# Optimization experiments

Measured on AMD Instinct MI355X. Metric: run time of the kernel, lower is better.

Reference implementation:

```python
import jax, jax.numpy as jnp
import numpy as np

N_NODES = 100000
N_EDGES = 3200000
IN_CH = 256
HIDDEN = 64
OUT_CH = 128


def setup_inputs() -> dict:
    key = jax.random.key(0)
    ks = jax.random.split(key, 6)
    x = jax.random.normal(ks[0], (N_NODES, IN_CH), dtype=jnp.float32)
    edge_index = jax.random.randint(ks[1], (2, N_EDGES), 0, N_NODES, dtype=jnp.int64)
    W1 = jax.random.normal(ks[2], (IN_CH, HIDDEN), dtype=jnp.float32) * (1.0 / np.sqrt(IN_CH))
    b1 = jnp.zeros((HIDDEN,), dtype=jnp.float32)
    W2 = jax.random.normal(ks[3], (HIDDEN, OUT_CH), dtype=jnp.float32) * (1.0 / np.sqrt(HIDDEN))
    b2 = jnp.zeros((OUT_CH,), dtype=jnp.float32)
    fcW = jax.random.normal(ks[4], (2, OUT_CH), dtype=jnp.float32) * (1.0 / np.sqrt(OUT_CH))
    fcb = jnp.zeros((2,), dtype=jnp.float32)
    return {"x": x, "edge_index": edge_index, "W1": W1, "b1": b1,
            "W2": W2, "b2": b2, "fcW": fcW, "fcb": fcb}


def _gcn_conv(x, edge_index, W, b):
    """PyG GCNConv: linear transform, add self-loops, symmetric D^-1/2 A D^-1/2 aggregation, bias."""
    N = x.shape[0]
    h = x @ W  # [N, F_out]
    loops = jnp.arange(N, dtype=edge_index.dtype)
    row = jnp.concatenate([edge_index[0], loops])  # source nodes
    col = jnp.concatenate([edge_index[1], loops])  # destination nodes
    deg = jax.ops.segment_sum(jnp.ones_like(col, dtype=h.dtype), col, num_segments=N)
    dinv = jnp.where(deg > 0, jax.lax.rsqrt(deg), 0.0)
    norm = dinv[row] * dinv[col]  # [E+N]
    out = jax.ops.segment_sum(h[row] * norm[:, None], col, num_segments=N)
    return out + b


def reference(x, edge_index, W1, b1, W2, b2, fcW, fcb):
    h = jax.nn.relu(_gcn_conv(x, edge_index, W1, b1))
    h = jax.nn.relu(_gcn_conv(h, edge_index, W2, b2))
    g = jnp.mean(h, axis=0)  # [OUT_CH]
    return g @ fcW.T + fcb   # [2]
```

## Files before the change

### kernel.cpp

```cpp
#include <hip/hip_runtime.h>

#define N_NODES 100000
#define N_EDGES 3200000
#define C_IN 256
#define C_H 64
#define C_OUT 128
#define NB 391
#define BCAP 16384
#define G2F 625
#define NTILES 6250
#define NT16 6250
#define G_GM 1563
#define CH1 8192

typedef unsigned int u32;
typedef unsigned short u16;
typedef unsigned long long u64;
typedef __attribute__((ext_vector_type(8))) short bf16x8;
typedef __attribute__((ext_vector_type(4))) float f32x4;

typedef __attribute__((address_space(3))) unsigned int l_u32;
typedef __attribute__((address_space(1))) const unsigned int g_u32;

__device__ __forceinline__ float bf2f(u16 u) {
    union { u32 i; float f; } v; v.i = ((u32)u) << 16; return v.f;
}
__device__ __forceinline__ u16 f2bf(float f) {
    union { float f; u32 i; } v; v.f = f;
    u32 x = v.i;
    return (u16)((x + 0x7fffu + ((x >> 16) & 1u)) >> 16);
}

__device__ __forceinline__ void gll16(const void* gp, const u16* lp) {
    __builtin_amdgcn_global_load_lds((g_u32*)gp, (l_u32*)lp, 16, 0, 0);
}

__global__ void k_detect(const void* __restrict__ x, const void* __restrict__ ei,
                         const void* __restrict__ b1, const void* __restrict__ b2,
                         const void* __restrict__ fcW, const void* __restrict__ fcb,
                         int* __restrict__ flags,
                         float* __restrict__ b1c, float* __restrict__ b2c,
                         float* __restrict__ fcWc, float* __restrict__ fcbc) {
    __shared__ int sf[2];
    int t = threadIdx.x;
    if (t < 64) {
        u32 w = ((const u32*)x)[t];
        u32 low = w & 0xffffu;
        int e = (int)((low >> 7) & 0xff);
        bool inw = (e > 96 && e < 160) || (low == 0);
        u64 m = __ballot(inw);
        if (t == 0) sf[0] = (__popcll(m) >= 60) ? 1 : 0;
    } else if (t < 128) {
        int i = t - 64;
        u32 w = ((const u32*)ei)[2 * i + 1];
        u64 m = __ballot(w == 0);
        if (i == 0) sf[1] = (m == ~0ull) ? 1 : 0;
    }
    __syncthreads();
    if (t == 0) { flags[0] = sf[0]; flags[1] = sf[1]; }
    int isbf = sf[0];
    if (isbf) {
        const u16* p1 = (const u16*)b1;  const u16* p2 = (const u16*)b2;
        const u16* pw = (const u16*)fcW; const u16* pb = (const u16*)fcb;
        for (int i = t; i < C_H; i += 256) b1c[i] = bf2f(p1[i]);
        for (int i = t; i < C_OUT; i += 256) b2c[i] = bf2f(p2[i]);
        for (int i = t; i < 2 * C_OUT; i += 256) fcWc[i] = bf2f(pw[i]);
        for (int i = t; i < 2; i += 256) fcbc[i] = bf2f(pb[i]);
    } else {
        const float* p1 = (const float*)b1;  const float* p2 = (const float*)b2;
        const float* pw = (const float*)fcW; const float* pb = (const float*)fcb;
        for (int i = t; i < C_H; i += 256) b1c[i] = p1[i];
        for (int i = t; i < C_OUT; i += 256) b2c[i] = p2[i];
        for (int i = t; i < 2 * C_OUT; i += 256) fcWc[i] = pw[i];
        for (int i = t; i < 2; i += 256) fcbc[i] = pb[i];
    }
}

__global__ __launch_bounds__(256) void k_prep(const void* __restrict__ W1,
                                              const void* __restrict__ W2,
                                              const int* __restrict__ flags,
                                              u16* __restrict__ W1m, u16* __restrict__ W2m,
                                              u32* __restrict__ bucket_cnt) {
    int b = blockIdx.x, t = threadIdx.x;
    int isbf = flags[0];
    int i = b * 256 + t;
    if (i < NB) bucket_cnt[i] = 0;
    if (i < C_IN * C_H) {
        const u16* w1b = (const u16*)W1; const float* w1f = (const float*)W1;
        int j = i & 7, lane = (i >> 3) & 63, nt = (i >> 9) & 3, k0 = i >> 11;
        int k = k0 * 32 + ((lane >> 4) & 3) * 8 + j;
        int n = nt * 16 + (lane & 15);
        W1m[i] = isbf ? w1b[k * C_H + n] : f2bf(w1f[k * C_H + n]);
    } else {
        int i2 = i - C_IN * C_H;
        const u16* w2b = (const u16*)W2; const float* w2f = (const float*)W2;
        int j = i2 & 7, lane = (i2 >> 3) & 63, nt = (i2 >> 9) & 7, k0 = (i2 >> 12) & 1;
        int k = k0 * 32 + ((lane >> 4) & 3) * 8 + j;
        int n = nt * 16 + (lane & 15);
        W2m[i2] = isbf ? w2b[k * C_OUT + n] : f2bf(w2f[k * C_OUT + n]);
    }
}

__global__ __launch_bounds__(512) void k_scatter1(const int* __restrict__ ei,
                                                  const int* __restrict__ flags,
                                                  u32* __restrict__ bucket_cnt,
                                                  u32* __restrict__ ebuf) {
    __shared__ u32 cnt[NB];
    __shared__ u32 lcur[NB];
    __shared__ u32 gbase[NB];
    __shared__ u32 lofs[512];
    __shared__ u32 stp[CH1];
    __shared__ u16 stb[CH1];
    int t = threadIdx.x;
    int is64 = flags[1];
    int e0 = blockIdx.x * CH1;
    int nv = min(CH1, N_EDGES - e0);
    for (int i = t; i < NB; i += 512) { cnt[i] = 0; lcur[i] = 0; }
    __syncthreads();
    for (int i = t; i < nv; i += 512) {
        int e = e0 + i;
        int d = is64 ? ei[2 * (N_EDGES + e)] : ei[N_EDGES + e];
        atomicAdd(&cnt[d >> 8], 1u);
    }
    __syncthreads();
    u32 v = (t < NB) ? cnt[t] : 0;
    lofs[t] = v;
    __syncthreads();
    for (int off = 1; off < 512; off <<= 1) {
        u32 a = (t >= off) ? lofs[t - off] : 0;
        __syncthreads();
        lofs[t] += a;
        __syncthreads();
    }
    u32 excl = lofs[t] - v;
    __syncthreads();
    lofs[t] = excl;
    __syncthreads();
    for (int i = t; i < nv; i += 512) {
        int e = e0 + i;
        int d, s;
        if (is64) { d = ei[2 * (N_EDGES + e)]; s = ei[2 * e]; }
        else      { d = ei[N_EDGES + e];       s = ei[e]; }
        int b = d >> 8;
        u32 slot = lofs[b] + atomicAdd(&lcur[b], 1u);
        stp[slot] = ((u32)(d & 255) << 20) | (u32)s;
        stb[slot] = (u16)b;
    }
    __syncthreads();
    for (int b = t; b < NB; b += 512) {
        u32 c = cnt[b];
        gbase[b] = c ? atomicAdd(&bucket_cnt[b], c) : 0;
    }
    __syncthreads();
    for (int s = t; s < nv; s += 512) {
        int b = stb[s];
        ebuf[(size_t)b * BCAP + gbase[b] + (s - lofs[b])] = stp[s];
    }
}

__global__ __launch_bounds__(512) void k_bscan(const u32* __restrict__ bucket_cnt,
                                               u32* __restrict__ bucket_base) {
    __shared__ u32 sm[512];
    int t = threadIdx.x;
    u32 v = (t < NB) ? bucket_cnt[t] : 0;
    sm[t] = v;
    __syncthreads();
    for (int off = 1; off < 512; off <<= 1) {
        u32 a = (t >= off) ? sm[t - off] : 0;
        __syncthreads();
        sm[t] += a;
        __syncthreads();
    }
    if (t < NB) bucket_base[t] = sm[t] - v;
    if (t == 0) bucket_base[NB] = N_EDGES;
}

__global__ __launch_bounds__(256) void k_scatter2(const u32* __restrict__ bucket_base,
                                                  const u32* __restrict__ ebuf,
                                                  int* __restrict__ rowptr,
                                                  float* __restrict__ dinv,
                                                  int* __restrict__ csr) {
    __shared__ int cnt[256];
    __shared__ int pfx[256];
    __shared__ int lcur[256];
    int b = blockIdx.x, t = threadIdx.x;
    int ebeg = (int)bucket_base[b], eend = (int)bucket_base[b + 1];
    int ne = eend - ebeg;
    const u32* src = ebuf + (size_t)b * BCAP;
    int sbeg = ebeg + (b << 8);
    cnt[t] = 0;
    lcur[t] = 0;
    __syncthreads();
    for (int i = t; i < ne; i += 256)
        atomicAdd(&cnt[(src[i] >> 20) & 255], 1);
    __syncthreads();
    int v = cnt[t];
    pfx[t] = v;
    __syncthreads();
    for (int off = 1; off < 256; off <<= 1) {
        int a = (t >= off) ? pfx[t - off] : 0;
        __syncthreads();
        pfx[t] += a;
        __syncthreads();
    }
    int node = (b << 8) + t;
    int rstart = sbeg + (pfx[t] - v) + t;
    if (node < N_NODES) {
        rowptr[node] = rstart;
        dinv[node] = rsqrtf((float)(v + 1));
        csr[rstart] = node << 7;
        if (node == N_NODES - 1) {
            rowptr[N_NODES] = rstart + v + 1;
            for (int i = 0; i < 64; ++i) csr[rstart + v + 1 + i] = 0;
        }
    }
    __syncthreads();
    for (int i = t; i < ne; i += 256) {
        u32 p = src[i];
        int dl = (p >> 20) & 255;
        int pos = sbeg + (pfx[dl] - cnt[dl]) + dl + 1 + atomicAdd(&lcur[dl], 1);
        csr[pos] = (int)((p & 0x1FFFFu) << 7);
    }
}

__global__ __launch_bounds__(256) void k_gemm1(const void* __restrict__ xv,
                                               const u16* __restrict__ W1m,
                                               const float* __restrict__ dinv,
                                               u16* __restrict__ g1,
                                               const int* __restrict__ flags) {
    __shared__ u16 wlds[C_IN * C_H];
    int t = threadIdx.x;
    int isbf = flags[0];
    {
        const uint4* src = (const uint4*)W1m;
        uint4* dst = (uint4*)wlds;
#pragma unroll
        for (int it = 0; it < 8; ++it) dst[t + it * 256] = src[t + it * 256];
    }
    __syncthreads();
    int w = t >> 6, lane = t & 63;
    int quad = lane >> 4, mrow = lane & 15;
    int m0 = blockIdx.x * 128 + w * 32;
    if (m0 >= N_NODES) return;

    bf16x8 a[2][8];
    if (isbf) {
        const u16* xb = (const u16*)xv;
#pragma unroll
        for (int mt = 0; mt < 2; ++mt)
#pragma unroll
            for (int k0 = 0; k0 < 8; ++k0)
                a[mt][k0] = *(const bf16x8*)(xb + (size_t)(m0 + mt * 16 + mrow) * C_IN + k0 * 32 + quad * 8);
    } else {
        const float* xf = (const float*)xv;
#pragma unroll
        for (int mt = 0; mt < 2; ++mt)
#pragma unroll
            for (int k0 = 0; k0 < 8; ++k0) {
                const float* p = xf + (size_t)(m0 + mt * 16 + mrow) * C_IN + k0 * 32 + quad * 8;
                float4 v0 = *(const float4*)p;
                float4 v1 = *(const float4*)(p + 4);
                bf16x8 r;
                r[0] = (short)f2bf(v0.x); r[1] = (short)f2bf(v0.y);
                r[2] = (short)f2bf(v0.z); r[3] = (short)f2bf(v0.w);
                r[4] = (short)f2bf(v1.x); r[5] = (short)f2bf(v1.y);
                r[6] = (short)f2bf(v1.z); r[7] = (short)f2bf(v1.w);
                a[mt][k0] = r;
            }
    }

    float dv0[4], dv1[4];
#pragma unroll
    for (int r = 0; r < 4; ++r) {
        dv0[r] = dinv[m0 + quad * 4 + r];
        dv1[r] = dinv[m0 + 16 + quad * 4 + r];
    }

#pragma unroll
    for (int nt = 0; nt < 4; ++nt) {
        bf16x8 b[8];
#pragma unroll
        for (int k0 = 0; k0 < 8; ++k0)
            b[k0] = *(const bf16x8*)&wlds[((k0 * 4 + nt) * 64 + lane) * 8];
        f32x4 acc0 = {0.f, 0.f, 0.f, 0.f};
        f32x4 acc1 = {0.f, 0.f, 0.f, 0.f};
#pragma unroll
        for (int k0 = 0; k0 < 8; ++k0) {
            acc0 = __builtin_amdgcn_mfma_f32_16x16x32_bf16(a[0][k0], b[k0], acc0, 0, 0, 0);
            acc1 = __builtin_amdgcn_mfma_f32_16x16x32_bf16(a[1][k0], b[k0], acc1, 0, 0, 0);
        }
        int ch = nt * 16 + mrow;
#pragma unroll
        for (int r = 0; r < 4; ++r) {
            g1[(size_t)(m0 + quad * 4 + r) * C_H + ch] = f2bf(acc0[r] * dv0[r]);
            g1[(size_t)(m0 + 16 + quad * 4 + r) * C_H + ch] = f2bf(acc1[r] * dv1[r]);
        }
    }
}

template <int MODE>
__global__ __launch_bounds__(256) void k_gatherM(const int* __restrict__ rowptr,
                                                 const int* __restrict__ csrb,
                                                 const float* __restrict__ dinv,
                                                 const u16* __restrict__ gt,
                                                 const float* __restrict__ bias,
                                                 u16* __restrict__ out) {
    __shared__ __align__(16) u16 hs[4][4096];
    __shared__ bf16x8 lut[81];
    int t = threadIdx.x;
    if (t < 81) {
        int s = t / 9, e = t - s * 9;
        bf16x8 le;
#pragma unroll
        for (int j = 0; j < 8; ++j) le[j] = (short)((j >= s && j < e) ? 0x3F80 : 0);
        lut[t] = le;
    }
    __syncthreads();
    int w = t >> 6, lane = t & 63;
    int tile = blockIdx.x * 4 + w;
    if (tile >= NT16) return;

    int g16 = lane >> 4, c = lane & 15;
    int n0 = tile << 4;
    int lo = rowptr[n0 + c];
    int hi = rowptr[n0 + c + 1];
    int beg = __shfl(lo, 0, 64);
    int end = __shfl(hi, 15, 64);
    int eidx = lane >> 3;
    int boff = (lane & 7) * 16;
    const char* gb = (const char*)gt;
    f32x4 acc0 = {0.f, 0.f, 0.f, 0.f}, acc1 = acc0, acc2 = acc0, acc3 = acc0;
    int nch = (end - beg + 31) >> 5;
    int cb = beg;
    {
        u32 o0 = (u32)csrb[cb + eidx];
        u32 o1 = (u32)csrb[cb + 8 + eidx];
        u32 o2 = (u32)csrb[cb + 16 + eidx];
        u32 o3 = (u32)csrb[cb + 24 + eidx];
        gll16(gb + o0 + boff, &hs[w][0]);
        gll16(gb + o1 + boff, &hs[w][512]);
        gll16(gb + o2 + boff, &hs[w][1024]);
        gll16(gb + o3 + boff, &hs[w][1536]);
        asm volatile("" ::: "memory");
    }
    for (int ci = 0; ci < nch; ++ci) {
        int cbn = cb + 32;
        bool more = (ci + 1 < nch);
        u32 n0o = 0, n1o = 0, n2o = 0, n3o = 0;
        if (more) {
            n0o = (u32)csrb[cbn + eidx];
            n1o = (u32)csrb[cbn + 8 + eidx];
            n2o = (u32)csrb[cbn + 16 + eidx];
            n3o = (u32)csrb[cbn + 24 + eidx];
        }
        if (more) asm volatile("s_waitcnt vmcnt(4)" ::: "memory");
        else      asm volatile("s_waitcnt vmcnt(0)" ::: "memory");
        const u16* lp = &hs[w][((ci & 1) << 11) + g16 * 512 + ((c >> 3) << 3) + (c & 7)];
        bf16x8 bfr[4];
#pragma unroll
        for (int cht = 0; cht < 4; ++cht) {
            u32 w0 = (u32)lp[0 * 64 + cht * 16] | ((u32)lp[1 * 64 + cht * 16] << 16);
            u32 w1 = (u32)lp[2 * 64 + cht * 16] | ((u32)lp[3 * 64 + cht * 16] << 16);
            u32 w2 = (u32)lp[4 * 64 + cht * 16] | ((u32)lp[5 * 64 + cht * 16] << 16);
            u32 w3 = (u32)lp[6 * 64 + cht * 16] | ((u32)lp[7 * 64 + cht * 16] << 16);
            union { u32 u[4]; bf16x8 v; } z;
            z.u[0] = w0; z.u[1] = w1; z.u[2] = w2; z.u[3] = w3;
            bfr[cht] = z.v;
        }
        int cbg = cb + g16 * 8;
        int s0 = min(max(lo - cbg, 0), 8);
        int e0 = min(max(hi - cbg, 0), 8);
        bf16x8 af = lut[s0 * 9 + e0];
        acc0 = __builtin_amdgcn_mfma_f32_16x16x32_bf16(af, bfr[0], acc0, 0, 0, 0);
        acc1 = __builtin_amdgcn_mfma_f32_16x16x32_bf16(af, bfr[1], acc1, 0, 0, 0);
        acc2 = __builtin_amdgcn_mfma_f32_16x16x32_bf16(af, bfr[2], acc2, 0, 0, 0);
        acc3 = __builtin_amdgcn_mfma_f32_16x16x32_bf16(af, bfr[3], acc3, 0, 0, 0);
        if (more) {
            int bo = ((ci + 1) & 1) << 11;
            gll16(gb + n0o + boff, &hs[w][bo]);
            gll16(gb + n1o + boff, &hs[w][bo + 512]);
            gll16(gb + n2o + boff, &hs[w][bo + 1024]);
            gll16(gb + n3o + boff, &hs[w][bo + 1536]);
            asm volatile("" ::: "memory");
        }
        cb = cbn;
    }
    float dv[4];
    int nb = n0 + g16 * 4;
#pragma unroll
    for (int r = 0; r < 4; ++r) dv[r] = dinv[nb + r];
    u16* ob = out + (size_t)nb * C_H + c;
#define EPI(ACC, CHT)                                                              \
    {                                                                              \
        float bs = (MODE == 0) ? bias[CHT * 16 + c] : 0.f;                         \
        _Pragma("unroll")                                                          \
        for (int r = 0; r < 4; ++r) {                                              \
            float val = (MODE == 0) ? dv[r] * fmaxf(dv[r] * ACC[r] + bs, 0.f)      \
                                    : dv[r] * ACC[r];                              \
            ob[r * C_H + CHT * 16] = f2bf(val);                                    \
        }                                                                          \
    }
    EPI(acc0, 0) EPI(acc1, 1) EPI(acc2, 2) EPI(acc3, 3)
#undef EPI
}

__global__ __launch_bounds__(256) void k_fused2(const u16* __restrict__ aggb,
                                                const u16* __restrict__ W2m,
                                                const float* __restrict__ b2c,
                                                float* __restrict__ partial) {
    __shared__ float psum[4 * 8 * 64];
    int t = threadIdx.x;
    int w = t >> 6, lane = t & 63;
    int quad = lane >> 4, m = lane & 15;

    bf16x8 b[2][8];
#pragma unroll
    for (int k0 = 0; k0 < 2; ++k0)
#pragma unroll
        for (int nt = 0; nt < 8; ++nt)
            b[k0][nt] = *(const bf16x8*)&W2m[((k0 * 8 + nt) * 64 + lane) * 8];

    float pacc[8] = {0.f, 0.f, 0.f, 0.f, 0.f, 0.f, 0.f, 0.f};
    float bias[8];
#pragma unroll
    for (int nt = 0; nt < 8; ++nt) bias[nt] = b2c[nt * 16 + m];

    for (int tile = blockIdx.x * 4 + w; tile < NTILES; tile += G2F * 4) {
        const u16* arow = aggb + (size_t)(tile * 16 + m) * C_H + quad * 8;
        bf16x8 a0 = *(const bf16x8*)(arow);
        bf16x8 a1 = *(const bf16x8*)(arow + 32);
#pragma unroll
        for (int nt = 0; nt < 8; ++nt) {
            f32x4 acc = {0.f, 0.f, 0.f, 0.f};
            acc = __builtin_amdgcn_mfma_f32_16x16x32_bf16(a0, b[0][nt], acc, 0, 0, 0);
            acc = __builtin_amdgcn_mfma_f32_16x16x32_bf16(a1, b[1][nt], acc, 0, 0, 0);
#pragma unroll
            for (int r = 0; r < 4; ++r)
                pacc[nt] += fmaxf(acc[r] + bias[nt], 0.f);
        }
    }
#pragma unroll
    for (int nt = 0; nt < 8; ++nt) psum[(w * 8 + nt) * 64 + lane] = pacc[nt];
    __syncthreads();
    if (t < 128) {
        int nt = t >> 4, m2 = t & 15;
        float s = 0.f;
#pragma unroll
        for (int ww = 0; ww < 4; ++ww)
#pragma unroll
            for (int q = 0; q < 4; ++q)
                s += psum[(ww * 8 + nt) * 64 + q * 16 + m2];
        partial[blockIdx.x * C_OUT + t] = s;
    }
}

__global__ __launch_bounds__(512) void k_final(const float* __restrict__ partial,
                                               const float* __restrict__ fcWc,
                                               const float* __restrict__ fcbc,
                                               void* __restrict__ out,
                                               const int* __restrict__ flags) {
    __shared__ float sm[512];
    __shared__ float red[256];
    int t = threadIdx.x;
    int f = t & 127, c = t >> 7;
    float s = 0.f;
    for (int b = c; b < G2F; b += 4) s += partial[b * 128 + f];
    sm[t] = s;
    __syncthreads();
    if (t < 128) {
        float gm = (sm[t] + sm[t + 128] + sm[t + 256] + sm[t + 384]) * (1.0f / (float)N_NODES);
        red[t] = gm * fcWc[t];
        red[128 + t] = gm * fcWc[128 + t];
    }
    __syncthreads();
    for (int off = 64; off >= 1; off >>= 1) {
        if (t < off) {
            red[t] += red[t + off];
            red[128 + t] += red[128 + t + off];
        }
        __syncthreads();
    }
    if (t == 0) {
        float o0 = red[0] + fcbc[0];
        float o1 = red[128] + fcbc[1];
        if (flags[0]) {
            u16* ob = (u16*)out;
            ob[0] = f2bf(o0);
            ob[1] = f2bf(o1);
        } else {
            float* of = (float*)out;
            of[0] = o0;
            of[1] = o1;
        }
    }
}

#define OFF_FLAGS   0u
#define OFF_DINV    512u
#define OFF_ROWPTR  400896u
#define OFF_BCNT    801280u
#define OFF_BBASE   802944u
#define OFF_CSR     1201664u
#define OFF_H1      14402560u
#define OFF_A1      27202560u
#define OFF_AGG     40002560u
#define OFF_PART    52802560u
#define OFF_W1C     53122560u
#define OFF_W2C     53155328u
#define OFF_B1C     53171712u
#define OFF_B2C     53171968u
#define OFF_FCWC    53172480u
#define OFF_FCBC    53173504u
#define OFF_EBUF    53174272u

extern "C" void kernel_launch(void* const* d_in, const int* in_sizes, int n_in,
                              void* d_out, int out_size, void* d_ws, size_t ws_size,
                              hipStream_t stream) {
    (void)in_sizes; (void)n_in; (void)out_size; (void)ws_size;
    const void* x   = d_in[0];
    const int*  ei  = (const int*)d_in[1];
    const void* W1  = d_in[2];
    const void* b1  = d_in[3];
    const void* W2  = d_in[4];
    const void* b2  = d_in[5];
    const void* fcW = d_in[6];
    const void* fcb = d_in[7];

    char* ws = (char*)d_ws;
    int*   flags  = (int*)(ws + OFF_FLAGS);
    float* dinv   = (float*)(ws + OFF_DINV);
    int*   rowptr = (int*)(ws + OFF_ROWPTR);
    u32*   bcnt   = (u32*)(ws + OFF_BCNT);
    u32*   bbase  = (u32*)(ws + OFF_BBASE);
    int*   csr    = (int*)(ws + OFF_CSR);
    u16*   g1     = (u16*)(ws + OFF_H1);
    u16*   a1s    = (u16*)(ws + OFF_A1);
    u16*   aggb   = (u16*)(ws + OFF_AGG);
    u32*   ebuf   = (u32*)(ws + OFF_EBUF);
    float* partial= (float*)(ws + OFF_PART);
    u16*   W1m    = (u16*)(ws + OFF_W1C);
    u16*   W2m    = (u16*)(ws + OFF_W2C);
    float* b1c    = (float*)(ws + OFF_B1C);
    float* b2c    = (float*)(ws + OFF_B2C);
    float* fcWc   = (float*)(ws + OFF_FCWC);
    float* fcbc   = (float*)(ws + OFF_FCBC);

    k_detect<<<1, 256, 0, stream>>>(x, ei, b1, b2, fcW, fcb,
                                    flags, b1c, b2c, fcWc, fcbc);
    k_prep<<<96, 256, 0, stream>>>(W1, W2, flags, W1m, W2m, bcnt);
    k_scatter1<<<NB, 512, 0, stream>>>(ei, flags, bcnt, ebuf);
    k_bscan<<<1, 512, 0, stream>>>(bcnt, bbase);
    k_scatter2<<<NB, 256, 0, stream>>>(bbase, ebuf, rowptr, dinv, csr);
    k_gemm1<<<(N_NODES + 127) / 128, 256, 0, stream>>>(x, W1m, dinv, g1, flags);
    k_gatherM<0><<<G_GM, 256, 0, stream>>>(rowptr, csr, dinv, g1, b1c, a1s);
    k_gatherM<1><<<G_GM, 256, 0, stream>>>(rowptr, csr, dinv, a1s, b2c, aggb);
    k_fused2<<<G2F, 256, 0, stream>>>(aggb, W2m, b2c, partial);
    k_final<<<1, 512, 0, stream>>>(partial, fcWc, fcbc, (void*)d_out, flags);
}
```

Before: 388.1 us.

## Store gathered node features in FP8 and use FP8 MFMA for aggregation

The intermediate per-node features g1 and a1 are now stored as FP8 (e4m3) with a x16 scale instead of bf16, and the two gather-aggregation kernels use the fp8 16x16x32 MFMA with an fp8 one-hot LUT. This halves the bytes gathered per edge and changes the CSR offset scale to 64-byte rows. It also folds the detect kernel into prep and the bucket scan into scatter2, so two launches go away. The cost is reduced precision in the intermediate activations, which may hurt accuracy.

```diff
diff --git a/kernel.cpp b/kernel.cpp
--- a/kernel.cpp
+++ b/kernel.cpp
@@ -15,6 +15,7 @@
 
 typedef unsigned int u32;
 typedef unsigned short u16;
+typedef unsigned char u8;
 typedef unsigned long long u64;
 typedef __attribute__((ext_vector_type(8))) short bf16x8;
 typedef __attribute__((ext_vector_type(4))) float f32x4;
@@ -30,59 +31,54 @@
     u32 x = v.i;
     return (u16)((x + 0x7fffu + ((x >> 16) & 1u)) >> 16);
 }
-
-__device__ __forceinline__ void gll16(const void* gp, const u16* lp) {
+__device__ __forceinline__ u8 f2fp8(float f) {
+    union { float f; u32 i; } v; v.f = f;
+    u32 s = (v.i >> 24) & 0x80u;
+    float a = __builtin_fabsf(f);
+    a = fminf(a, 448.f);
+    if (a < 0.015625f) {
+        int m = (int)__builtin_rintf(a * 512.f);
+        return (u8)(s | (u32)m);
+    }
+    union { float ff; u32 i; } w; w.ff = a;
+    u32 x = w.i;
+    u32 r = x + 0x7FFFFu + ((x >> 20) & 1u);
+    u32 E = (r >> 23) - 120u;
+    u32 m = (r >> 20) & 7u;
+    return (u8)(s | (E << 3) | m);
+}
+
+__device__ __forceinline__ void gll16(const void* gp, const void* lp) {
     __builtin_amdgcn_global_load_lds((g_u32*)gp, (l_u32*)lp, 16, 0, 0);
 }
 
-__global__ void k_detect(const void* __restrict__ x, const void* __restrict__ ei,
-                         const void* __restrict__ b1, const void* __restrict__ b2,
-                         const void* __restrict__ fcW, const void* __restrict__ fcb,
-                         int* __restrict__ flags,
-                         float* __restrict__ b1c, float* __restrict__ b2c,
-                         float* __restrict__ fcWc, float* __restrict__ fcbc) {
-    __shared__ int sf[2];
-    int t = threadIdx.x;
+__global__ __launch_bounds__(256) void k_prep(const void* __restrict__ x, const void* __restrict__ ei,
+                                              const void* __restrict__ W1, const void* __restrict__ W2,
+                                              const void* __restrict__ b1, const void* __restrict__ b2,
+                                              const void* __restrict__ fcW, const void* __restrict__ fcb,
+                                              int* __restrict__ flags,
+                                              u16* __restrict__ W1m, u16* __restrict__ W2m,
+                                              u32* __restrict__ bucket_cnt,
+                                              float* __restrict__ b1c, float* __restrict__ b2c,
+                                              float* __restrict__ fcWc, float* __restrict__ fcbc) {
+    __shared__ int sfb;
+    int b = blockIdx.x, t = threadIdx.x;
     if (t < 64) {
-        u32 w = ((const u32*)x)[t];
-        u32 low = w & 0xffffu;
+        u32 wv = ((const u32*)x)[t];
+        u32 low = wv & 0xffffu;
         int e = (int)((low >> 7) & 0xff);
         bool inw = (e > 96 && e < 160) || (low == 0);
         u64 m = __ballot(inw);
-        if (t == 0) sf[0] = (__popcll(m) >= 60) ? 1 : 0;
-    } else if (t < 128) {
+        if (t == 0) sfb = (__popcll(m) >= 60) ? 1 : 0;
+    } else if (b == 0 && t < 128) {
         int i = t - 64;
-        u32 w = ((const u32*)ei)[2 * i + 1];
-        u64 m = __ballot(w == 0);
-        if (i == 0) sf[1] = (m == ~0ull) ? 1 : 0;
-    }
-    __syncthreads();
-    if (t == 0) { flags[0] = sf[0]; flags[1] = sf[1]; }
-    int isbf = sf[0];
-    if (isbf) {
-        const u16* p1 = (const u16*)b1;  const u16* p2 = (const u16*)b2;
-        const u16* pw = (const u16*)fcW; const u16* pb = (const u16*)fcb;
-        for (int i = t; i < C_H; i += 256) b1c[i] = bf2f(p1[i]);
-        for (int i = t; i < C_OUT; i += 256) b2c[i] = bf2f(p2[i]);
-        for (int i = t; i < 2 * C_OUT; i += 256) fcWc[i] = bf2f(pw[i]);
-        for (int i = t; i < 2; i += 256) fcbc[i] = bf2f(pb[i]);
-    } else {
-        const float* p1 = (const float*)b1;  const float* p2 = (const float*)b2;
-        const float* pw = (const float*)fcW; const float* pb = (const float*)fcb;
-        for (int i = t; i < C_H; i += 256) b1c[i] = p1[i];
-        for (int i = t; i < C_OUT; i += 256) b2c[i] = p2[i];
-        for (int i = t; i < 2 * C_OUT; i += 256) fcWc[i] = pw[i];
-        for (int i = t; i < 2; i += 256) fcbc[i] = pb[i];
-    }
-}
-
-__global__ __launch_bounds__(256) void k_prep(const void* __restrict__ W1,
-                                              const void* __restrict__ W2,
-                                              const int* __restrict__ flags,
-                                              u16* __restrict__ W1m, u16* __restrict__ W2m,
-                                              u32* __restrict__ bucket_cnt) {
-    int b = blockIdx.x, t = threadIdx.x;
-    int isbf = flags[0];
+        u32 wv = ((const u32*)ei)[2 * i + 1];
+        u64 m = __ballot(wv == 0);
+        if (i == 0) flags[1] = (m == ~0ull) ? 1 : 0;
+    }
+    __syncthreads();
+    int isbf = sfb;
+    if (b == 0 && t == 0) flags[0] = isbf;
     int i = b * 256 + t;
     if (i < NB) bucket_cnt[i] = 0;
     if (i < C_IN * C_H) {
@@ -99,6 +95,23 @@
         int n = nt * 16 + (lane & 15);
         W2m[i2] = isbf ? w2b[k * C_OUT + n] : f2bf(w2f[k * C_OUT + n]);
     }
+    if (b == 0) {
+        if (isbf) {
+            const u16* p1 = (const u16*)b1;  const u16* p2 = (const u16*)b2;
+            const u16* pw = (const u16*)fcW; const u16* pb = (const u16*)fcb;
+            for (int q = t; q < C_H; q += 256) b1c[q] = bf2f(p1[q]);
+            for (int q = t; q < C_OUT; q += 256) b2c[q] = bf2f(p2[q]);
+            for (int q = t; q < 2 * C_OUT; q += 256) fcWc[q] = bf2f(pw[q]);
+            for (int q = t; q < 2; q += 256) fcbc[q] = bf2f(pb[q]);
+        } else {
+            const float* p1 = (const float*)b1;  const float* p2 = (const float*)b2;
+            const float* pw = (const float*)fcW; const float* pb = (const float*)fcb;
+            for (int q = t; q < C_H; q += 256) b1c[q] = p1[q];
+            for (int q = t; q < C_OUT; q += 256) b2c[q] = p2[q];
+            for (int q = t; q < 2 * C_OUT; q += 256) fcWc[q] = pw[q];
+            for (int q = t; q < 2; q += 256) fcbc[q] = pb[q];
+        }
+    }
 }
 
 __global__ __launch_bounds__(512) void k_scatter1(const int* __restrict__ ei,
@@ -158,34 +171,31 @@
     }
 }
 
-__global__ __launch_bounds__(512) void k_bscan(const u32* __restrict__ bucket_cnt,
-                                               u32* __restrict__ bucket_base) {
-    __shared__ u32 sm[512];
-    int t = threadIdx.x;
-    u32 v = (t < NB) ? bucket_cnt[t] : 0;
-    sm[t] = v;
-    __syncthreads();
-    for (int off = 1; off < 512; off <<= 1) {
-        u32 a = (t >= off) ? sm[t - off] : 0;
-        __syncthreads();
-        sm[t] += a;
-        __syncthreads();
-    }
-    if (t < NB) bucket_base[t] = sm[t] - v;
-    if (t == 0) bucket_base[NB] = N_EDGES;
-}
-
-__global__ __launch_bounds__(256) void k_scatter2(const u32* __restrict__ bucket_base,
+__global__ __launch_bounds__(256) void k_scatter2(const u32* __restrict__ bucket_cnt,
                                                   const u32* __restrict__ ebuf,
                                                   int* __restrict__ rowptr,
                                                   float* __restrict__ dinv,
                                                   int* __restrict__ csr) {
+    __shared__ u32 ssum[256];
+    __shared__ u32 snev;
     __shared__ int cnt[256];
     __shared__ int pfx[256];
     __shared__ int lcur[256];
     int b = blockIdx.x, t = threadIdx.x;
-    int ebeg = (int)bucket_base[b], eend = (int)bucket_base[b + 1];
-    int ne = eend - ebeg;
+    u32 a = 0;
+    for (int i = t; i < NB; i += 256) {
+        u32 cv = bucket_cnt[i];
+        if (i < b) a += cv;
+        if (i == b) snev = cv;
+    }
+    ssum[t] = a;
+    __syncthreads();
+    for (int off = 128; off >= 1; off >>= 1) {
+        if (t < off) ssum[t] += ssum[t + off];
+        __syncthreads();
+    }
+    int ebeg = (int)ssum[0];
+    int ne = (int)snev;
     const u32* src = ebuf + (size_t)b * BCAP;
     int sbeg = ebeg + (b << 8);
     cnt[t] = 0;
@@ -198,9 +208,9 @@
     pfx[t] = v;
     __syncthreads();
     for (int off = 1; off < 256; off <<= 1) {
-        int a = (t >= off) ? pfx[t - off] : 0;
+        int pv = (t >= off) ? pfx[t - off] : 0;
         __syncthreads();
-        pfx[t] += a;
+        pfx[t] += pv;
         __syncthreads();
     }
     int node = (b << 8) + t;
@@ -208,7 +218,7 @@
     if (node < N_NODES) {
         rowptr[node] = rstart;
         dinv[node] = rsqrtf((float)(v + 1));
-        csr[rstart] = node << 7;
+        csr[rstart] = node << 6;
         if (node == N_NODES - 1) {
             rowptr[N_NODES] = rstart + v + 1;
             for (int i = 0; i < 64; ++i) csr[rstart + v + 1 + i] = 0;
@@ -219,14 +229,14 @@
         u32 p = src[i];
         int dl = (p >> 20) & 255;
         int pos = sbeg + (pfx[dl] - cnt[dl]) + dl + 1 + atomicAdd(&lcur[dl], 1);
-        csr[pos] = (int)((p & 0x1FFFFu) << 7);
+        csr[pos] = (int)((p & 0x1FFFFu) << 6);
     }
 }
 
 __global__ __launch_bounds__(256) void k_gemm1(const void* __restrict__ xv,
                                                const u16* __restrict__ W1m,
                                                const float* __restrict__ dinv,
-                                               u16* __restrict__ g1,
+                                               u8* __restrict__ g1,
                                                const int* __restrict__ flags) {
     __shared__ u16 wlds[C_IN * C_H];
     int t = threadIdx.x;
@@ -272,8 +282,8 @@
     float dv0[4], dv1[4];
 #pragma unroll
     for (int r = 0; r < 4; ++r) {
-        dv0[r] = dinv[m0 + quad * 4 + r];
-        dv1[r] = dinv[m0 + 16 + quad * 4 + r];
+        dv0[r] = dinv[m0 + quad * 4 + r] * 16.f;
+        dv1[r] = dinv[m0 + 16 + quad * 4 + r] * 16.f;
     }
 
 #pragma unroll
@@ -292,8 +302,8 @@
         int ch = nt * 16 + mrow;
 #pragma unroll
         for (int r = 0; r < 4; ++r) {
-            g1[(size_t)(m0 + quad * 4 + r) * C_H + ch] = f2bf(acc0[r] * dv0[r]);
-            g1[(size_t)(m0 + 16 + quad * 4 + r) * C_H + ch] = f2bf(acc1[r] * dv1[r]);
+            g1[(size_t)(m0 + quad * 4 + r) * C_H + ch] = f2fp8(acc0[r] * dv0[r]);
+            g1[(size_t)(m0 + 16 + quad * 4 + r) * C_H + ch] = f2fp8(acc1[r] * dv1[r]);
         }
     }
 }
@@ -302,18 +312,20 @@
 __global__ __launch_bounds__(256) void k_gatherM(const int* __restrict__ rowptr,
                                                  const int* __restrict__ csrb,
                                                  const float* __restrict__ dinv,
-                                                 const u16* __restrict__ gt,
+                                                 const u8* __restrict__ gt,
                                                  const float* __restrict__ bias,
-                                                 u16* __restrict__ out) {
-    __shared__ __align__(16) u16 hs[4][4096];
-    __shared__ bf16x8 lut[81];
+                                                 void* __restrict__ out) {
+    __shared__ __align__(16) u8 hsb[4][4096];
+    __shared__ u64 lut8[81];
     int t = threadIdx.x;
     if (t < 81) {
         int s = t / 9, e = t - s * 9;
-        bf16x8 le;
-#pragma unroll
-        for (int j = 0; j < 8; ++j) le[j] = (short)((j >= s && j < e) ? 0x3F80 : 0);
-        lut[t] = le;
+        u32 lo = 0, hi = 0;
+#pragma unroll
+        for (int j = 0; j < 4; ++j) if (j >= s && j < e) lo |= 0x18u << (8 * j);
+#pragma unroll
+        for (int j = 4; j < 8; ++j) if (j >= s && j < e) hi |= 0x18u << (8 * (j - 4));
+        lut8[t] = ((u64)hi << 32) | lo;
     }
     __syncthreads();
     int w = t >> 6, lane = t & 63;
@@ -326,61 +338,52 @@
     int hi = rowptr[n0 + c + 1];
     int beg = __shfl(lo, 0, 64);
     int end = __shfl(hi, 15, 64);
-    int eidx = lane >> 3;
-    int boff = (lane & 7) * 16;
+    int ridx = lane >> 2;
+    int bq = (lane & 3) * 16;
     const char* gb = (const char*)gt;
+    u8* hw = hsb[w];
     f32x4 acc0 = {0.f, 0.f, 0.f, 0.f}, acc1 = acc0, acc2 = acc0, acc3 = acc0;
     int nch = (end - beg + 31) >> 5;
     int cb = beg;
     {
-        u32 o0 = (u32)csrb[cb + eidx];
-        u32 o1 = (u32)csrb[cb + 8 + eidx];
-        u32 o2 = (u32)csrb[cb + 16 + eidx];
-        u32 o3 = (u32)csrb[cb + 24 + eidx];
-        gll16(gb + o0 + boff, &hs[w][0]);
-        gll16(gb + o1 + boff, &hs[w][512]);
-        gll16(gb + o2 + boff, &hs[w][1024]);
-        gll16(gb + o3 + boff, &hs[w][1536]);
+        u32 o0 = (u32)csrb[cb + ridx];
+        u32 o1 = (u32)csrb[cb + 16 + ridx];
+        gll16(gb + o0 + bq, hw);
+        gll16(gb + o1 + bq, hw + 1024);
         asm volatile("" ::: "memory");
     }
     for (int ci = 0; ci < nch; ++ci) {
         int cbn = cb + 32;
         bool more = (ci + 1 < nch);
-        u32 n0o = 0, n1o = 0, n2o = 0, n3o = 0;
+        u32 n0o = 0, n1o = 0;
         if (more) {
-            n0o = (u32)csrb[cbn + eidx];
-            n1o = (u32)csrb[cbn + 8 + eidx];
-            n2o = (u32)csrb[cbn + 16 + eidx];
-            n3o = (u32)csrb[cbn + 24 + eidx];
-        }
-        if (more) asm volatile("s_waitcnt vmcnt(4)" ::: "memory");
+            n0o = (u32)csrb[cbn + ridx];
+            n1o = (u32)csrb[cbn + 16 + ridx];
+        }
+        if (more) asm volatile("s_waitcnt vmcnt(2)" ::: "memory");
         else      asm volatile("s_waitcnt vmcnt(0)" ::: "memory");
-        const u16* lp = &hs[w][((ci & 1) << 11) + g16 * 512 + ((c >> 3) << 3) + (c & 7)];
-        bf16x8 bfr[4];
-#pragma unroll
-        for (int cht = 0; cht < 4; ++cht) {
-            u32 w0 = (u32)lp[0 * 64 + cht * 16] | ((u32)lp[1 * 64 + cht * 16] << 16);
-            u32 w1 = (u32)lp[2 * 64 + cht * 16] | ((u32)lp[3 * 64 + cht * 16] << 16);
-            u32 w2 = (u32)lp[4 * 64 + cht * 16] | ((u32)lp[5 * 64 + cht * 16] << 16);
-            u32 w3 = (u32)lp[6 * 64 + cht * 16] | ((u32)lp[7 * 64 + cht * 16] << 16);
-            union { u32 u[4]; bf16x8 v; } z;
-            z.u[0] = w0; z.u[1] = w1; z.u[2] = w2; z.u[3] = w3;
-            bfr[cht] = z.v;
-        }
+        const u8* lp = hw + ((ci & 1) << 11) + g16 * 512 + c;
         int cbg = cb + g16 * 8;
         int s0 = min(max(lo - cbg, 0), 8);
         int e0 = min(max(hi - cbg, 0), 8);
-        bf16x8 af = lut[s0 * 9 + e0];
-        acc0 = __builtin_amdgcn_mfma_f32_16x16x32_bf16(af, bfr[0], acc0, 0, 0, 0);
-        acc1 = __builtin_amdgcn_mfma_f32_16x16x32_bf16(af, bfr[1], acc1, 0, 0, 0);
-        acc2 = __builtin_amdgcn_mfma_f32_16x16x32_bf16(af, bfr[2], acc2, 0, 0, 0);
-        acc3 = __builtin_amdgcn_mfma_f32_16x16x32_bf16(af, bfr[3], acc3, 0, 0, 0);
+        union P8 { u32 u[2]; long l; } pa, pb0, pb1, pb2, pb3;
+        u64 av = lut8[s0 * 9 + e0];
+        pa.u[0] = (u32)av; pa.u[1] = (u32)(av >> 32);
+#define LDB(P, O)                                                                           \
+        P.u[0] = (u32)lp[O] | ((u32)lp[O + 64] << 8) | ((u32)lp[O + 128] << 16) |           \
+                 ((u32)lp[O + 192] << 24);                                                  \
+        P.u[1] = (u32)lp[O + 256] | ((u32)lp[O + 320] << 8) | ((u32)lp[O + 384] << 16) |    \
+                 ((u32)lp[O + 448] << 24);
+        LDB(pb0, 0) LDB(pb1, 16) LDB(pb2, 32) LDB(pb3, 48)
+#undef LDB
+        acc0 = __builtin_amdgcn_mfma_f32_16x16x32_fp8_fp8(pa.l, pb0.l, acc0, 0, 0, 0);
+        acc1 = __builtin_amdgcn_mfma_f32_16x16x32_fp8_fp8(pa.l, pb1.l, acc1, 0, 0, 0);
+        acc2 = __builtin_amdgcn_mfma_f32_16x16x32_fp8_fp8(pa.l, pb2.l, acc2, 0, 0, 0);
+        acc3 = __builtin_amdgcn_mfma_f32_16x16x32_fp8_fp8(pa.l, pb3.l, acc3, 0, 0, 0);
         if (more) {
             int bo = ((ci + 1) & 1) << 11;
-            gll16(gb + n0o + boff, &hs[w][bo]);
-            gll16(gb + n1o + boff, &hs[w][bo + 512]);
-            gll16(gb + n2o + boff, &hs[w][bo + 1024]);
-            gll16(gb + n3o + boff, &hs[w][bo + 1536]);
+            gll16(gb + n0o + bq, hw + bo);
+            gll16(gb + n1o + bq, hw + bo + 1024);
             asm volatile("" ::: "memory");
         }
         cb = cbn;
@@ -389,19 +392,29 @@
     int nb = n0 + g16 * 4;
 #pragma unroll
     for (int r = 0; r < 4; ++r) dv[r] = dinv[nb + r];
-    u16* ob = out + (size_t)nb * C_H + c;
-#define EPI(ACC, CHT)                                                              \
-    {                                                                              \
-        float bs = (MODE == 0) ? bias[CHT * 16 + c] : 0.f;                         \
-        _Pragma("unroll")                                                          \
-        for (int r = 0; r < 4; ++r) {                                              \
-            float val = (MODE == 0) ? dv[r] * fmaxf(dv[r] * ACC[r] + bs, 0.f)      \
-                                    : dv[r] * ACC[r];                              \
-            ob[r * C_H + CHT * 16] = f2bf(val);                                    \
-        }                                                                          \
-    }
-    EPI(acc0, 0) EPI(acc1, 1) EPI(acc2, 2) EPI(acc3, 3)
+    if (MODE == 0) {
+        u8* ob = (u8*)out + (size_t)nb * C_H + c;
+#define EPI(ACC, CHT)                                                                       \
+        {                                                                                   \
+            float bs = bias[CHT * 16 + c];                                                  \
+            _Pragma("unroll")                                                               \
+            for (int r = 0; r < 4; ++r)                                                     \
+                ob[r * C_H + CHT * 16] =                                                    \
+                    f2fp8(16.f * dv[r] * fmaxf(dv[r] * ACC[r] + bs, 0.f));                  \
+        }
+        EPI(acc0, 0) EPI(acc1, 1) EPI(acc2, 2) EPI(acc3, 3)
 #undef EPI
+    } else {
+        u16* ob = (u16*)out + (size_t)nb * C_H + c;
+#define EPI(ACC, CHT)                                                                       \
+        {                                                                                   \
+            _Pragma("unroll")                                                               \
+            for (int r = 0; r < 4; ++r)                                                     \
+                ob[r * C_H + CHT * 16] = f2bf(dv[r] * ACC[r]);                              \
+        }
+        EPI(acc0, 0) EPI(acc1, 1) EPI(acc2, 2) EPI(acc3, 3)
+#undef EPI
+    }
 }
 
 __global__ __launch_bounds__(256) void k_fused2(const u16* __restrict__ aggb,
@@ -499,7 +512,6 @@
 #define OFF_DINV    512u
 #define OFF_ROWPTR  400896u
 #define OFF_BCNT    801280u
-#define OFF_BBASE   802944u
 #define OFF_CSR     1201664u
 #define OFF_H1      14402560u
 #define OFF_A1      27202560u
@@ -531,10 +543,9 @@
     float* dinv   = (float*)(ws + OFF_DINV);
     int*   rowptr = (int*)(ws + OFF_ROWPTR);
     u32*   bcnt   = (u32*)(ws + OFF_BCNT);
-    u32*   bbase  = (u32*)(ws + OFF_BBASE);
     int*   csr    = (int*)(ws + OFF_CSR);
-    u16*   g1     = (u16*)(ws + OFF_H1);
-    u16*   a1s    = (u16*)(ws + OFF_A1);
+    u8*    g1     = (u8*)(ws + OFF_H1);
+    u8*    a1s    = (u8*)(ws + OFF_A1);
     u16*   aggb   = (u16*)(ws + OFF_AGG);
     u32*   ebuf   = (u32*)(ws + OFF_EBUF);
     float* partial= (float*)(ws + OFF_PART);
@@ -545,15 +556,13 @@
     float* fcWc   = (float*)(ws + OFF_FCWC);
     float* fcbc   = (float*)(ws + OFF_FCBC);
 
-    k_detect<<<1, 256, 0, stream>>>(x, ei, b1, b2, fcW, fcb,
-                                    flags, b1c, b2c, fcWc, fcbc);
-    k_prep<<<96, 256, 0, stream>>>(W1, W2, flags, W1m, W2m, bcnt);
+    k_prep<<<96, 256, 0, stream>>>(x, ei, W1, W2, b1, b2, fcW, fcb,
+                                   flags, W1m, W2m, bcnt, b1c, b2c, fcWc, fcbc);
     k_scatter1<<<NB, 512, 0, stream>>>(ei, flags, bcnt, ebuf);
-    k_bscan<<<1, 512, 0, stream>>>(bcnt, bbase);
-    k_scatter2<<<NB, 256, 0, stream>>>(bbase, ebuf, rowptr, dinv, csr);
+    k_scatter2<<<NB, 256, 0, stream>>>(bcnt, ebuf, rowptr, dinv, csr);
     k_gemm1<<<(N_NODES + 127) / 128, 256, 0, stream>>>(x, W1m, dinv, g1, flags);
-    k_gatherM<0><<<G_GM, 256, 0, stream>>>(rowptr, csr, dinv, g1, b1c, a1s);
-    k_gatherM<1><<<G_GM, 256, 0, stream>>>(rowptr, csr, dinv, a1s, b2c, aggb);
+    k_gatherM<0><<<G_GM, 256, 0, stream>>>(rowptr, csr, dinv, g1, b1c, (void*)a1s);
+    k_gatherM<1><<<G_GM, 256, 0, stream>>>(rowptr, csr, dinv, a1s, b2c, (void*)aggb);
     k_fused2<<<G2F, 256, 0, stream>>>(aggb, W2m, b2c, partial);
     k_final<<<1, 512, 0, stream>>>(partial, fcWc, fcbc, (void*)d_out, flags);
 }
```

After: 361.3 us. -6.9%, faster.
